# Optimization experiments

Hardware: AMD Instinct MI355X
Metric: run time of the kernel (lower is better)

## Reference

```python
import jax, jax.numpy as jnp
import numpy as np

N = 50000      # nodes
E = 600000     # edges
F_IN = 128     # num_node_features
H = 128        # hidden_channels
C = 10         # num_classes
G = 512        # graphs in batch
EPS = 1e-5


def setup_inputs() -> dict:
    key = jax.random.key(0)
    ks = jax.random.split(key, 12)
    x = jax.random.normal(ks[0], (N, F_IN), dtype=jnp.float32)
    edge_index = jax.random.randint(ks[1], (2, E), 0, N, dtype=jnp.int32)
    batch = jnp.sort(jax.random.randint(ks[2], (N,), 0, G, dtype=jnp.int32))
    s_in = 1.0 / np.sqrt(F_IN)
    s_h = 1.0 / np.sqrt(H)
    W1 = jax.random.uniform(ks[3], (H, F_IN), jnp.float32, -s_in, s_in)
    b1 = jax.random.uniform(ks[4], (H,), jnp.float32, -s_in, s_in)
    W2 = jax.random.uniform(ks[5], (H, H), jnp.float32, -s_h, s_h)
    b2 = jax.random.uniform(ks[6], (H,), jnp.float32, -s_h, s_h)
    W3 = jax.random.uniform(ks[7], (H, H), jnp.float32, -s_h, s_h)
    b3 = jax.random.uniform(ks[8], (H,), jnp.float32, -s_h, s_h)
    Wlin = jax.random.uniform(ks[9], (C, H), jnp.float32, -s_h, s_h)
    blin = jax.random.uniform(ks[10], (C,), jnp.float32, -s_h, s_h)
    return {"x": x, "edge_index": edge_index, "batch": batch,
            "W1": W1, "b1": b1, "W2": W2, "b2": b2, "W3": W3, "b3": b3,
            "Wlin": Wlin, "blin": blin}


def _gcn_norm(edge_index, num_nodes):
    # PyG GCNConv default: add self-loops, symmetric D^-1/2 A D^-1/2 norm
    loop = jnp.arange(num_nodes, dtype=edge_index.dtype)
    src = jnp.concatenate([edge_index[0], loop])
    dst = jnp.concatenate([edge_index[1], loop])
    deg = jax.ops.segment_sum(jnp.ones_like(dst, dtype=jnp.float32), dst,
                              num_segments=num_nodes)
    dinv = jnp.where(deg > 0, jax.lax.rsqrt(deg), 0.0)
    norm = dinv[src] * dinv[dst]  # [E+N]
    return src, dst, norm


def _gcn_conv(x, W, b, src, dst, norm, num_nodes):
    h = x @ W.T                                  # [N, H]
    msg = norm[:, None] * h[src]                 # gather: [E+N, H]
    out = jax.ops.segment_sum(msg, dst, num_segments=num_nodes)  # scatter-add
    return out + b


def _batchnorm(x):
    # BatchNorm1d(affine=False), training mode: batch stats, biased variance
    mu = jnp.mean(x, axis=0)
    var = jnp.mean(jnp.square(x - mu), axis=0)
    return (x - mu) * jax.lax.rsqrt(var + EPS)


def reference(x, edge_index, batch, W1, b1, W2, b2, W3, b3, Wlin, blin):
    src, dst, norm = _gcn_norm(edge_index, N)
    h = _gcn_conv(x, W1, b1, src, dst, norm, N)
    h = jax.nn.relu(_batchnorm(h))
    h = _gcn_conv(h, W2, b2, src, dst, norm, N)
    h = jax.nn.relu(_batchnorm(h))
    h = _gcn_conv(h, W3, b3, src, dst, norm, N)
    # global mean pool over graphs
    sums = jax.ops.segment_sum(h, batch, num_segments=G)
    cnts = jax.ops.segment_sum(jnp.ones((N,), jnp.float32), batch, num_segments=G)
    pooled = sums / jnp.maximum(cnts, 1.0)[:, None]   # [G, H]
    return pooled @ Wlin.T + blin                     # [G, C]
```

## Files before the change

### kernel.cpp

```cpp
#include <hip/hip_runtime.h>
#include <hip/hip_bf16.h>

#define NN 50000
#define NE 600000
#define FD 128
#define NG 512
#define NC 10
static constexpr float EPS_BN = 1e-5f;

typedef __bf16 bf16x8 __attribute__((ext_vector_type(8)));
typedef float f32x4 __attribute__((ext_vector_type(4)));

__device__ __forceinline__ unsigned short f2bf(float x) {
  unsigned u = __float_as_uint(x);
  u = (u + 0x7FFFu + ((u >> 16) & 1u)) >> 16;
  return (unsigned short)u;
}
__device__ __forceinline__ float bf2f(unsigned short h) {
  return __uint_as_float(((unsigned)h) << 16);
}

__global__ __launch_bounds__(256) void k_zero(float4* __restrict__ p) {
  int i = blockIdx.x * 256 + threadIdx.x;
  if (i < 13536) p[i] = make_float4(0.f, 0.f, 0.f, 0.f);
}

#define FILL_CHUNKS 293
#define GRID_E8 (8 * FILL_CHUNKS)
#define DRANGE 6250
__global__ __launch_bounds__(256) void k_deg_scatter(const int* __restrict__ dst, float* __restrict__ deg) {
  int b = blockIdx.x, t = threadIdx.x;
  int g = b & 7;
  int chunk = b >> 3;
  int dlo = g * DRANGE, dhi = dlo + DRANGE;
  int e0 = chunk * 2048;
#pragma unroll
  for (int i = 0; i < 8; ++i) {
    int e = e0 + i * 256 + t;
    if (e < NE) {
      int d = dst[e];
      if (d >= dlo && d < dhi) unsafeAtomicAdd(&deg[d], 1.0f);
    }
  }
}

#define NB 196
__global__ __launch_bounds__(256) void k_bsum(const float* __restrict__ deg, int* __restrict__ bsum) {
  __shared__ int s[256];
  int t = threadIdx.x, i = blockIdx.x * 256 + t;
  s[t] = (i < NN) ? (int)deg[i] : 0;
  __syncthreads();
  for (int o = 128; o > 0; o >>= 1) { if (t < o) s[t] += s[t + o]; __syncthreads(); }
  if (t == 0) bsum[blockIdx.x] = s[0];
}

__global__ __launch_bounds__(256) void k_bscan(const int* __restrict__ bsum, int* __restrict__ bbase) {
  __shared__ int s[256];
  int t = threadIdx.x;
  int v = (t < NB) ? bsum[t] : 0;
  s[t] = v; __syncthreads();
  for (int o = 1; o < 256; o <<= 1) {
    int a = (t >= o) ? s[t - o] : 0; __syncthreads();
    s[t] += a; __syncthreads();
  }
  if (t < NB) bbase[t] = s[t] - v;
}

__global__ __launch_bounds__(256) void k_rowoff_cvt(float* __restrict__ deg, const int* __restrict__ bbase,
                                                    int* __restrict__ row_off, int* __restrict__ cursor,
                                                    const float* __restrict__ W1, const float* __restrict__ W2,
                                                    const float* __restrict__ W3, unsigned short* __restrict__ w2,
                                                    const int* __restrict__ batch, int* __restrict__ gstart) {
  int b = blockIdx.x, t = threadIdx.x;
  if (b < NB) {
    __shared__ int s[256];
    int i = b * 256 + t;
    float dv = (i < NN) ? deg[i] : 0.f;
    int c = (int)dv;
    s[t] = c; __syncthreads();
    for (int o = 1; o < 256; o <<= 1) {
      int a = (t >= o) ? s[t - o] : 0; __syncthreads();
      s[t] += a; __syncthreads();
    }
    int excl = s[t] - c + bbase[b];
    if (i <= NN) {
      row_off[i] = excl;
      if (i < NN) {
        cursor[i] = excl;
        deg[i] = rsqrtf(dv + 1.0f);
      }
    }
  } else if (b < NB + 48) {
    int bb = b - NB;
    int m = bb >> 4;
    const float* W = (m == 0) ? W1 : ((m == 1) ? W2 : W3);
    int i = (bb & 15) * 256 + t;
    float4 v = ((const float4*)W)[i];
    ushort4 hv;
    hv.x = f2bf(v.x); hv.y = f2bf(v.y); hv.z = f2bf(v.z); hv.w = f2bf(v.w);
    int e0 = i * 4, row = e0 >> 7, col = e0 & 127;
    int sc_ = ((col & 120) ^ ((row & 7) << 3)) | (col & 7);
    *(ushort4*)(w2 + m * FD * FD + row * FD + sc_) = hv;
  } else {
    int g = (b - NB - 48) * 256 + t;
    if (g > NG) return;
    int lo = 0, hi = NN;
    while (lo < hi) {
      int mid = (lo + hi) >> 1;
      if (batch[mid] < g) lo = mid + 1; else hi = mid;
    }
    gstart[g] = lo;
  }
}

__global__ __launch_bounds__(256) void k_fill(const int* __restrict__ src, const int* __restrict__ dst,
                                              const float* __restrict__ dinv, int* __restrict__ cursor,
                                              int2* __restrict__ csr) {
  int b = blockIdx.x, t = threadIdx.x;
  int g = b & 7;
  int chunk = b >> 3;
  int dlo = g * DRANGE, dhi = dlo + DRANGE;
  int e0 = chunk * 2048;
#pragma unroll
  for (int i = 0; i < 8; ++i) {
    int e = e0 + i * 256 + t;
    if (e < NE) {
      int d = dst[e];
      if (d >= dlo && d < dhi) {
        int s = src[e];
        float nrm = dinv[s] * dinv[d];
        int pos = atomicAdd(&cursor[d], 1);
        csr[pos] = make_int2(s, __float_as_int(nrm));
      }
    }
  }
}

template <int BN, int F32IN>
__global__ __launch_bounds__(256) void k_gemm(const void* __restrict__ in, const float* __restrict__ bn8,
                                              const unsigned short* __restrict__ wsrc,
                                              unsigned short* __restrict__ hb) {
  __shared__ unsigned short w_lds[FD * FD];
  __shared__ float s_musc[2 * FD];
  int t = threadIdx.x;
  {
    const uint4* s4 = (const uint4*)wsrc;
    uint4* d4 = (uint4*)w_lds;
#pragma unroll
    for (int c = 0; c < 8; ++c) d4[c * 256 + t] = s4[c * 256 + t];
  }
  if constexpr (BN != 0) {
    if (t < FD) {
      float s = 0.f, q = 0.f;
#pragma unroll
      for (int c = 0; c < 8; ++c) { s += bn8[c * FD + t]; q += bn8[1024 + c * FD + t]; }
      float m = s * (1.0f / NN);
      float v = fmaxf(q * (1.0f / NN) - m * m, 0.f);
      s_musc[t] = m;
      s_musc[FD + t] = rsqrtf(v + EPS_BN);
    }
  }
  __syncthreads();

  int w = t >> 6, l = t & 63;
  int rt = blockIdx.x * 4 + w;
  if (rt >= NN / 16) return;
  int r = l & 15, g = l >> 4;
  int ko = g * 8;
  f32x4 acc[8];
#pragma unroll
  for (int ct = 0; ct < 8; ++ct) acc[ct] = (f32x4){0.f, 0.f, 0.f, 0.f};

#pragma unroll
  for (int kk = 0; kk < FD; kk += 32) {
    float a0[8];
    if constexpr (F32IN != 0) {
      const float* p0 = (const float*)in + (size_t)(rt * 16 + r) * FD + kk + ko;
      float4 x0 = *(const float4*)p0;
      float4 x1 = *(const float4*)(p0 + 4);
      a0[0] = x0.x; a0[1] = x0.y; a0[2] = x0.z; a0[3] = x0.w;
      a0[4] = x1.x; a0[5] = x1.y; a0[6] = x1.z; a0[7] = x1.w;
    } else {
      uint4 pv = *(const uint4*)((const unsigned short*)in + (size_t)(rt * 16 + r) * FD + kk + ko);
      a0[0] = __uint_as_float(pv.x << 16); a0[1] = __uint_as_float(pv.x & 0xffff0000u);
      a0[2] = __uint_as_float(pv.y << 16); a0[3] = __uint_as_float(pv.y & 0xffff0000u);
      a0[4] = __uint_as_float(pv.z << 16); a0[5] = __uint_as_float(pv.z & 0xffff0000u);
      a0[6] = __uint_as_float(pv.w << 16); a0[7] = __uint_as_float(pv.w & 0xffff0000u);
    }
    if constexpr (BN != 0) {
      const float* mp = s_musc + kk + ko;
      float4 m0 = *(const float4*)mp, m1 = *(const float4*)(mp + 4);
      float4 s0 = *(const float4*)(mp + FD), s1 = *(const float4*)(mp + FD + 4);
      float mu[8] = {m0.x, m0.y, m0.z, m0.w, m1.x, m1.y, m1.z, m1.w};
      float sc[8] = {s0.x, s0.y, s0.z, s0.w, s1.x, s1.y, s1.z, s1.w};
#pragma unroll
      for (int i = 0; i < 8; ++i)
        a0[i] = fmaxf((a0[i] - mu[i]) * sc[i], 0.f);
    }
    bf16x8 ah, al;
#pragma unroll
    for (int i = 0; i < 8; ++i) {
      __bf16 h0 = (__bf16)a0[i];
      ah[i] = h0; al[i] = (__bf16)(a0[i] - (float)h0);
    }
#pragma unroll
    for (int ct = 0; ct < 8; ++ct) {
      int row = ct * 16 + r;
      int idx = row * FD + ((kk + ko) ^ ((r & 7) << 3));
      bf16x8 bh = *(const bf16x8*)(w_lds + idx);
      acc[ct] = __builtin_amdgcn_mfma_f32_16x16x32_bf16(ah, bh, acc[ct], 0, 0, 0);
      acc[ct] = __builtin_amdgcn_mfma_f32_16x16x32_bf16(al, bh, acc[ct], 0, 0, 0);
    }
  }
#pragma unroll
  for (int ct = 0; ct < 8; ++ct)
#pragma unroll
    for (int i = 0; i < 4; ++i)
      hb[(size_t)(rt * 16 + g * 4 + i) * FD + ct * 16 + r] = f2bf(acc[ct][i]);
}

template <int STATS>
__global__ __launch_bounds__(256) void k_agg(const unsigned short* __restrict__ hb,
                                             const float* __restrict__ dinv,
                                             const float* __restrict__ bias, const int* __restrict__ row_off,
                                             const int2* __restrict__ csr, unsigned short* __restrict__ outb,
                                             float* __restrict__ bn8) {
  int t = threadIdx.x;
  int n = blockIdx.x * 16 + (t >> 4);
  int q = t & 15;
  const uint4* hb4 = (const uint4*)hb;
  float dv = dinv[n];
  float s2 = dv * dv;
  float4 acc0 = ((const float4*)bias)[q * 2];
  float4 acc1 = ((const float4*)bias)[q * 2 + 1];
  {
    uint4 pv = hb4[(size_t)n * 16 + q];
    acc0.x = fmaf(s2, __uint_as_float(pv.x << 16), acc0.x);
    acc0.y = fmaf(s2, __uint_as_float(pv.x & 0xffff0000u), acc0.y);
    acc0.z = fmaf(s2, __uint_as_float(pv.y << 16), acc0.z);
    acc0.w = fmaf(s2, __uint_as_float(pv.y & 0xffff0000u), acc0.w);
    acc1.x = fmaf(s2, __uint_as_float(pv.z << 16), acc1.x);
    acc1.y = fmaf(s2, __uint_as_float(pv.z & 0xffff0000u), acc1.y);
    acc1.z = fmaf(s2, __uint_as_float(pv.w << 16), acc1.z);
    acc1.w = fmaf(s2, __uint_as_float(pv.w & 0xffff0000u), acc1.w);
  }
  int lo = row_off[n], hi = row_off[n + 1];
  for (int j = lo; j < hi; ++j) {
    int2 e = csr[j];
    float w = __int_as_float(e.y);
    uint4 pv = hb4[(size_t)e.x * 16 + q];
    acc0.x = fmaf(w, __uint_as_float(pv.x << 16), acc0.x);
    acc0.y = fmaf(w, __uint_as_float(pv.x & 0xffff0000u), acc0.y);
    acc0.z = fmaf(w, __uint_as_float(pv.y << 16), acc0.z);
    acc0.w = fmaf(w, __uint_as_float(pv.y & 0xffff0000u), acc0.w);
    acc1.x = fmaf(w, __uint_as_float(pv.z << 16), acc1.x);
    acc1.y = fmaf(w, __uint_as_float(pv.z & 0xffff0000u), acc1.y);
    acc1.z = fmaf(w, __uint_as_float(pv.w << 16), acc1.z);
    acc1.w = fmaf(w, __uint_as_float(pv.w & 0xffff0000u), acc1.w);
  }
  {
    unsigned short o[8];
    o[0] = f2bf(acc0.x); o[1] = f2bf(acc0.y); o[2] = f2bf(acc0.z); o[3] = f2bf(acc0.w);
    o[4] = f2bf(acc1.x); o[5] = f2bf(acc1.y); o[6] = f2bf(acc1.z); o[7] = f2bf(acc1.w);
    *(uint4*)(outb + (size_t)n * FD + q * 8) = *(uint4*)o;
  }

  if constexpr (STATS != 0) {
    __shared__ float red_s[16][FD + 4], red_q[16][FD + 4];
    int slot = t >> 4, f = q * 8;
    red_s[slot][f + 0] = acc0.x; red_s[slot][f + 1] = acc0.y;
    red_s[slot][f + 2] = acc0.z; red_s[slot][f + 3] = acc0.w;
    red_s[slot][f + 4] = acc1.x; red_s[slot][f + 5] = acc1.y;
    red_s[slot][f + 6] = acc1.z; red_s[slot][f + 7] = acc1.w;
    red_q[slot][f + 0] = acc0.x * acc0.x; red_q[slot][f + 1] = acc0.y * acc0.y;
    red_q[slot][f + 2] = acc0.z * acc0.z; red_q[slot][f + 3] = acc0.w * acc0.w;
    red_q[slot][f + 4] = acc1.x * acc1.x; red_q[slot][f + 5] = acc1.y * acc1.y;
    red_q[slot][f + 6] = acc1.z * acc1.z; red_q[slot][f + 7] = acc1.w * acc1.w;
    __syncthreads();
    if (t < FD) {
      float s = 0.f, qq = 0.f;
#pragma unroll
      for (int m = 0; m < 16; ++m) { s += red_s[m][t]; qq += red_q[m][t]; }
      int c = (blockIdx.x & 7) * FD + t;
      unsafeAtomicAdd(&bn8[c], s);
      unsafeAtomicAdd(&bn8[1024 + c], qq);
    }
  }
}

__global__ __launch_bounds__(512) void k_poolfinal(const unsigned short* __restrict__ hbB,
                                                   const int* __restrict__ gstart,
                                                   const float* __restrict__ Wlin, const float* __restrict__ blin,
                                                   float* __restrict__ out) {
  __shared__ float ps[4][FD];
  __shared__ float pp[FD];
  int g = blockIdx.x, t = threadIdx.x;
  int part = t >> 7, f = t & 127;
  int lo = gstart[g], hi = gstart[g + 1];
  float s = 0.f;
  for (int n = lo + part; n < hi; n += 4) s += bf2f(hbB[(size_t)n * FD + f]);
  ps[part][f] = s;
  __syncthreads();
  if (t < FD) {
    float tot = ps[0][t] + ps[1][t] + ps[2][t] + ps[3][t];
    pp[t] = tot * (1.0f / fmaxf((float)(hi - lo), 1.0f));
  }
  __syncthreads();
  if (t < NC) {
    float a = blin[t];
    for (int k = 0; k < FD; ++k) a = fmaf(pp[k], Wlin[t * FD + k], a);
    out[g * NC + t] = a;
  }
}

extern "C" void kernel_launch(void* const* d_in, const int* in_sizes, int n_in,
                              void* d_out, int out_size, void* d_ws, size_t ws_size,
                              hipStream_t stream) {
  const float* x    = (const float*)d_in[0];
  const int*   ei   = (const int*)d_in[1];
  const int*   batch= (const int*)d_in[2];
  const float* W1   = (const float*)d_in[3];
  const float* b1   = (const float*)d_in[4];
  const float* W2   = (const float*)d_in[5];
  const float* b2   = (const float*)d_in[6];
  const float* W3   = (const float*)d_in[7];
  const float* b3   = (const float*)d_in[8];
  const float* Wlin = (const float*)d_in[9];
  const float* blin = (const float*)d_in[10];
  float* out = (float*)d_out;
  float* ws  = (float*)d_ws;

  const int* srcI = ei;
  const int* dstI = ei + NE;

  float* deg    = ws;
  float* bnA    = ws + 50048;
  float* bnB    = bnA + 2048;
  int2*  csr    = (int2*)(bnB + 2048);
  int*   row_off= (int*)(csr + NE);
  int*   cursor = row_off + 50048;
  int*   gstart = cursor + 50048;
  int*   bsum   = gstart + 1024;
  int*   bbase  = bsum + 256;
  unsigned short* w2  = (unsigned short*)(bbase + 256);
  unsigned short* hb  = w2 + 3 * FD * FD;
  unsigned short* hbB = hb + NN * FD;

  dim3 B(256);
  const int gGemm = (NN / 16 + 3) / 4;
  const int gAgg  = NN / 16;

  k_zero<<<53, B, 0, stream>>>((float4*)ws);
  k_deg_scatter<<<GRID_E8, B, 0, stream>>>(dstI, deg);
  k_bsum<<<NB, B, 0, stream>>>(deg, bsum);
  k_bscan<<<1, B, 0, stream>>>(bsum, bbase);
  k_rowoff_cvt<<<NB + 48 + 3, B, 0, stream>>>(deg, bbase, row_off, cursor,
                                              W1, W2, W3, w2, batch, gstart);
  k_fill<<<GRID_E8, B, 0, stream>>>(srcI, dstI, deg, cursor, csr);

  k_gemm<0, 1><<<gGemm, B, 0, stream>>>(x, nullptr, w2, hb);
  k_agg<1><<<gAgg, B, 0, stream>>>(hb, deg, b1, row_off, csr, hbB, bnA);

  k_gemm<1, 0><<<gGemm, B, 0, stream>>>(hbB, bnA, w2 + FD * FD, hb);
  k_agg<1><<<gAgg, B, 0, stream>>>(hb, deg, b2, row_off, csr, hbB, bnB);

  k_gemm<1, 0><<<gGemm, B, 0, stream>>>(hbB, bnB, w2 + 2 * FD * FD, hb);
  k_agg<0><<<gAgg, B, 0, stream>>>(hb, deg, b3, row_off, csr, hbB, nullptr);

  k_poolfinal<<<NG, 512, 0, stream>>>(hbB, gstart, Wlin, blin, out);
}
```

Before: 244.2 us.

## Factor symmetric GCN norm into GEMM epilogue and aggregation, shrink CSR to src-only

Splits the D^-1/2 A D^-1/2 normalization so the GEMM epilogue scales each row by dinv[src] and the aggregation scales the summed neighbours by dinv[dst]. The CSR no longer stores a per-edge weight, so it shrinks from int2 to int. This halves CSR traffic in the three aggregation passes and removes the dinv gathers in k_fill. The inner loop becomes plain adds. Rounding changes slightly because the scaled h is stored as bf16 before summation.

```diff
diff --git a/kernel.cpp b/kernel.cpp
--- a/kernel.cpp
+++ b/kernel.cpp
@@ -114,8 +114,7 @@
 }
 
 __global__ __launch_bounds__(256) void k_fill(const int* __restrict__ src, const int* __restrict__ dst,
-                                              const float* __restrict__ dinv, int* __restrict__ cursor,
-                                              int2* __restrict__ csr) {
+                                              int* __restrict__ cursor, int* __restrict__ csr_src) {
   int b = blockIdx.x, t = threadIdx.x;
   int g = b & 7;
   int chunk = b >> 3;
@@ -127,10 +126,8 @@
     if (e < NE) {
       int d = dst[e];
       if (d >= dlo && d < dhi) {
-        int s = src[e];
-        float nrm = dinv[s] * dinv[d];
         int pos = atomicAdd(&cursor[d], 1);
-        csr[pos] = make_int2(s, __float_as_int(nrm));
+        csr_src[pos] = src[e];
       }
     }
   }
@@ -139,6 +136,7 @@
 template <int BN, int F32IN>
 __global__ __launch_bounds__(256) void k_gemm(const void* __restrict__ in, const float* __restrict__ bn8,
                                               const unsigned short* __restrict__ wsrc,
+                                              const float* __restrict__ dinv,
                                               unsigned short* __restrict__ hb) {
   __shared__ unsigned short w_lds[FD * FD];
   __shared__ float s_musc[2 * FD];
@@ -212,70 +210,69 @@
       acc[ct] = __builtin_amdgcn_mfma_f32_16x16x32_bf16(al, bh, acc[ct], 0, 0, 0);
     }
   }
+  float dvr[4];
+#pragma unroll
+  for (int i = 0; i < 4; ++i) dvr[i] = dinv[rt * 16 + g * 4 + i];
 #pragma unroll
   for (int ct = 0; ct < 8; ++ct)
 #pragma unroll
     for (int i = 0; i < 4; ++i)
-      hb[(size_t)(rt * 16 + g * 4 + i) * FD + ct * 16 + r] = f2bf(acc[ct][i]);
+      hb[(size_t)(rt * 16 + g * 4 + i) * FD + ct * 16 + r] = f2bf(dvr[i] * acc[ct][i]);
 }
 
 template <int STATS>
 __global__ __launch_bounds__(256) void k_agg(const unsigned short* __restrict__ hb,
                                              const float* __restrict__ dinv,
                                              const float* __restrict__ bias, const int* __restrict__ row_off,
-                                             const int2* __restrict__ csr, unsigned short* __restrict__ outb,
+                                             const int* __restrict__ csr_src, unsigned short* __restrict__ outb,
                                              float* __restrict__ bn8) {
   int t = threadIdx.x;
   int n = blockIdx.x * 16 + (t >> 4);
   int q = t & 15;
   const uint4* hb4 = (const uint4*)hb;
-  float dv = dinv[n];
-  float s2 = dv * dv;
-  float4 acc0 = ((const float4*)bias)[q * 2];
-  float4 acc1 = ((const float4*)bias)[q * 2 + 1];
+  float4 acc0, acc1;
   {
     uint4 pv = hb4[(size_t)n * 16 + q];
-    acc0.x = fmaf(s2, __uint_as_float(pv.x << 16), acc0.x);
-    acc0.y = fmaf(s2, __uint_as_float(pv.x & 0xffff0000u), acc0.y);
-    acc0.z = fmaf(s2, __uint_as_float(pv.y << 16), acc0.z);
-    acc0.w = fmaf(s2, __uint_as_float(pv.y & 0xffff0000u), acc0.w);
-    acc1.x = fmaf(s2, __uint_as_float(pv.z << 16), acc1.x);
-    acc1.y = fmaf(s2, __uint_as_float(pv.z & 0xffff0000u), acc1.y);
-    acc1.z = fmaf(s2, __uint_as_float(pv.w << 16), acc1.z);
-    acc1.w = fmaf(s2, __uint_as_float(pv.w & 0xffff0000u), acc1.w);
+    acc0.x = __uint_as_float(pv.x << 16); acc0.y = __uint_as_float(pv.x & 0xffff0000u);
+    acc0.z = __uint_as_float(pv.y << 16); acc0.w = __uint_as_float(pv.y & 0xffff0000u);
+    acc1.x = __uint_as_float(pv.z << 16); acc1.y = __uint_as_float(pv.z & 0xffff0000u);
+    acc1.z = __uint_as_float(pv.w << 16); acc1.w = __uint_as_float(pv.w & 0xffff0000u);
   }
   int lo = row_off[n], hi = row_off[n + 1];
   for (int j = lo; j < hi; ++j) {
-    int2 e = csr[j];
-    float w = __int_as_float(e.y);
-    uint4 pv = hb4[(size_t)e.x * 16 + q];
-    acc0.x = fmaf(w, __uint_as_float(pv.x << 16), acc0.x);
-    acc0.y = fmaf(w, __uint_as_float(pv.x & 0xffff0000u), acc0.y);
-    acc0.z = fmaf(w, __uint_as_float(pv.y << 16), acc0.z);
-    acc0.w = fmaf(w, __uint_as_float(pv.y & 0xffff0000u), acc0.w);
-    acc1.x = fmaf(w, __uint_as_float(pv.z << 16), acc1.x);
-    acc1.y = fmaf(w, __uint_as_float(pv.z & 0xffff0000u), acc1.y);
-    acc1.z = fmaf(w, __uint_as_float(pv.w << 16), acc1.z);
-    acc1.w = fmaf(w, __uint_as_float(pv.w & 0xffff0000u), acc1.w);
-  }
+    int s = csr_src[j];
+    uint4 pv = hb4[(size_t)s * 16 + q];
+    acc0.x += __uint_as_float(pv.x << 16); acc0.y += __uint_as_float(pv.x & 0xffff0000u);
+    acc0.z += __uint_as_float(pv.y << 16); acc0.w += __uint_as_float(pv.y & 0xffff0000u);
+    acc1.x += __uint_as_float(pv.z << 16); acc1.y += __uint_as_float(pv.z & 0xffff0000u);
+    acc1.z += __uint_as_float(pv.w << 16); acc1.w += __uint_as_float(pv.w & 0xffff0000u);
+  }
+  float dv = dinv[n];
+  float4 b0 = ((const float4*)bias)[q * 2];
+  float4 b1v = ((const float4*)bias)[q * 2 + 1];
+  float4 o0, o1;
+  o0.x = fmaf(dv, acc0.x, b0.x); o0.y = fmaf(dv, acc0.y, b0.y);
+  o0.z = fmaf(dv, acc0.z, b0.z); o0.w = fmaf(dv, acc0.w, b0.w);
+  o1.x = fmaf(dv, acc1.x, b1v.x); o1.y = fmaf(dv, acc1.y, b1v.y);
+  o1.z = fmaf(dv, acc1.z, b1v.z); o1.w = fmaf(dv, acc1.w, b1v.w);
   {
     unsigned short o[8];
-    o[0] = f2bf(acc0.x); o[1] = f2bf(acc0.y); o[2] = f2bf(acc0.z); o[3] = f2bf(acc0.w);
-    o[4] = f2bf(acc1.x); o[5] = f2bf(acc1.y); o[6] = f2bf(acc1.z); o[7] = f2bf(acc1.w);
+    o[0] = f2bf(o0.x); o[1] = f2bf(o0.y); o[2] = f2bf(o0.z); o[3] = f2bf(o0.w);
+    o[4] = f2bf(o1.x); o[5] = f2bf(o1.y); o[6] = f2bf(o1.z); o[7] = f2bf(o1.w);
     *(uint4*)(outb + (size_t)n * FD + q * 8) = *(uint4*)o;
   }
 
   if constexpr (STATS != 0) {
     __shared__ float red_s[16][FD + 4], red_q[16][FD + 4];
     int slot = t >> 4, f = q * 8;
-    red_s[slot][f + 0] = acc0.x; red_s[slot][f + 1] = acc0.y;
-    red_s[slot][f + 2] = acc0.z; red_s[slot][f + 3] = acc0.w;
-    red_s[slot][f + 4] = acc1.x; red_s[slot][f + 5] = acc1.y;
-    red_s[slot][f + 6] = acc1.z; red_s[slot][f + 7] = acc1.w;
-    red_q[slot][f + 0] = acc0.x * acc0.x; red_q[slot][f + 1] = acc0.y * acc0.y;
-    red_q[slot][f + 2] = acc0.z * acc0.z; red_q[slot][f + 3] = acc0.w * acc0.w;
-    red_q[slot][f + 4] = acc1.x * acc1.x; red_q[slot][f + 5] = acc1.y * acc1.y;
-    red_q[slot][f + 6] = acc1.z * acc1.z; red_q[slot][f + 7] = acc1.w * acc1.w;
+    red_s[slot][f + 0] = o0.x; red_s[slot][f + 1] = o0.y;
+    red_s[slot][f + 2] = o0.z; red_s[slot][f + 3] = o0.w;
+    red_s[slot][f + 4] = o1.x; red_s[slot][f + 5] = o1.y;
+    red_s[slot][f + 6] = o1.z; red_s[slot][f + 7] = o1.w;
+    red_q[slot][f + 0] = o0.x * o0.x; red_q[slot][f + 1] = o0.y * o0.y;
+    red_q[slot][f + 2] = o0.z * o0.z; red_q[slot][f + 3] = o0.w * o0.w;
+    red_q[slot][f + 4] = o1.x * o1.x; red_q[slot][f + 5] = o1.y * o1.y;
+    red_q[slot][f + 6] = o1.z * o1.z; red_q[slot][f + 7] = o1.w * o1.w;
     __syncthreads();
     if (t < FD) {
       float s = 0.f, qq = 0.f;
@@ -336,8 +333,8 @@
   float* deg    = ws;
   float* bnA    = ws + 50048;
   float* bnB    = bnA + 2048;
-  int2*  csr    = (int2*)(bnB + 2048);
-  int*   row_off= (int*)(csr + NE);
+  int*   csr_src= (int*)(bnB + 2048);
+  int*   row_off= csr_src + NE;
   int*   cursor = row_off + 50048;
   int*   gstart = cursor + 50048;
   int*   bsum   = gstart + 1024;
@@ -356,16 +353,16 @@
   k_bscan<<<1, B, 0, stream>>>(bsum, bbase);
   k_rowoff_cvt<<<NB + 48 + 3, B, 0, stream>>>(deg, bbase, row_off, cursor,
                                               W1, W2, W3, w2, batch, gstart);
-  k_fill<<<GRID_E8, B, 0, stream>>>(srcI, dstI, deg, cursor, csr);
-
-  k_gemm<0, 1><<<gGemm, B, 0, stream>>>(x, nullptr, w2, hb);
-  k_agg<1><<<gAgg, B, 0, stream>>>(hb, deg, b1, row_off, csr, hbB, bnA);
-
-  k_gemm<1, 0><<<gGemm, B, 0, stream>>>(hbB, bnA, w2 + FD * FD, hb);
-  k_agg<1><<<gAgg, B, 0, stream>>>(hb, deg, b2, row_off, csr, hbB, bnB);
-
-  k_gemm<1, 0><<<gGemm, B, 0, stream>>>(hbB, bnB, w2 + 2 * FD * FD, hb);
-  k_agg<0><<<gAgg, B, 0, stream>>>(hb, deg, b3, row_off, csr, hbB, nullptr);
+  k_fill<<<GRID_E8, B, 0, stream>>>(srcI, dstI, cursor, csr_src);
+
+  k_gemm<0, 1><<<gGemm, B, 0, stream>>>(x, nullptr, w2, deg, hb);
+  k_agg<1><<<gAgg, B, 0, stream>>>(hb, deg, b1, row_off, csr_src, hbB, bnA);
+
+  k_gemm<1, 0><<<gGemm, B, 0, stream>>>(hbB, bnA, w2 + FD * FD, deg, hb);
+  k_agg<1><<<gAgg, B, 0, stream>>>(hb, deg, b2, row_off, csr_src, hbB, bnB);
+
+  k_gemm<1, 0><<<gGemm, B, 0, stream>>>(hbB, bnB, w2 + 2 * FD * FD, deg, hb);
+  k_agg<0><<<gAgg, B, 0, stream>>>(hb, deg, b3, row_off, csr_src, hbB, nullptr);
 
   k_poolfinal<<<NG, 512, 0, stream>>>(hbB, gstart, Wlin, blin, out);
 }
```

After: 238.2 us. -2.5%, faster.
